# Performance work log

Measured on AMD Instinct MI355X. Metric: run time of the kernel, lower is better.

Reference implementation:

```python
import jax, jax.numpy as jnp
import numpy as np

DIM = 1792      # 256+512+1024 = WRN50 layer1-3 channels
GAMMA_D = 1
K_TOP = 3
EPS = 0.1
MAX_ITER = 200
B, H, W = 2, 56, 56


def avg_pool3x3(x):
    # F.avg_pool2d(x, 3, 1, 1), count_include_pad=True -> always divide by 9
    s = jax.lax.reduce_window(x, 0.0, jax.lax.add, (1, 1, 3, 3), (1, 1, 1, 1),
                              [(0, 0), (0, 0), (1, 1), (1, 1)])
    return s / 9.0


def descriptor(p1, p2, p3, w_coord, b_coord, w_eca):
    sample = avg_pool3x3(p1)
    b, _, h, w = sample.shape
    for o in (p2, p3):
        o = avg_pool3x3(o)
        # F.interpolate(..., mode='bilinear', align_corners=False) == half-pixel bilinear
        o = jax.image.resize(o, (o.shape[0], o.shape[1], h, w), method='bilinear')
        sample = jnp.concatenate([sample, o], axis=1)      # [b,1792,h,w]
    # CoordConv2d(dim, dim//gamma_d, 1): append normalized coord channels, 1x1 conv
    xx = jnp.broadcast_to(jnp.linspace(-1.0, 1.0, w, dtype=sample.dtype)[None, None, None, :], (b, 1, h, w))
    yy = jnp.broadcast_to(jnp.linspace(-1.0, 1.0, h, dtype=sample.dtype)[None, None, :, None], (b, 1, h, w))
    z = jnp.concatenate([sample, xx, yy], axis=1)          # [b,1794,h,w]
    phi = jnp.einsum('bchw,oc->bohw', z, w_coord) + b_coord[None, :, None, None]
    # eca_layer(dim, k_size=9): GAP -> conv1d over channel axis -> sigmoid gate
    y = phi.mean(axis=(2, 3))                              # [b,C]
    y = jax.lax.conv_general_dilated(y[:, None, :], w_eca[None, None, :], (1,),
                                     [(4, 4)], dimension_numbers=('NCH', 'OIH', 'NCH'))[:, 0, :]
    gate = jax.nn.sigmoid(y)[:, :, None, None]
    return phi * (1.0 + 0.1 * gate)                        # 0.1*eca(phi) + phi


def sinkhorn(Ccost, mu, nu):
    # plain Sinkhorn (TopK_custom forward), 200 iterations
    G = jnp.exp(-Ccost / EPS)                              # [bs,n,m]
    bs, n, m = Ccost.shape

    def body(i, uv):
        u, v = uv
        u = mu / (G * v).sum(-1, keepdims=True)            # [bs,n,1]
        v = nu / (G * u).sum(-2, keepdims=True)            # [bs,1,m]
        return (u, v)

    u0 = jnp.ones((bs, n, 1), Ccost.dtype)
    v0 = jnp.ones((bs, 1, m), Ccost.dtype) / m
    u, v = jax.lax.fori_loop(0, MAX_ITER, body, (u0, v0))
    return u * G * v


def soft_topk(scores):
    # SOFT top-k via 2-anchor optimal transport; selects the K_TOP SMALLEST scores
    bs, n = scores.shape
    anchors = jnp.array([0.0, 1.0], scores.dtype)          # [selected, rest]
    Ccost = (scores[..., None] - anchors) ** 2             # [bs,n,2]
    Ccost = Ccost / jax.lax.stop_gradient(Ccost.max())
    mu = jnp.ones((1, n, 1), scores.dtype) / n
    nu = jnp.array([K_TOP / n, (n - K_TOP) / n], scores.dtype).reshape(1, 1, 2)
    Gamma = sinkhorn(Ccost, mu, nu)
    return Gamma[..., 0] * n                               # soft top-K membership mask


def adfa_forward(p1, p2, p3, w_coord, b_coord, w_eca, C):
    phi = descriptor(p1, p2, p3, w_coord, b_coord, w_eca)  # [b,c,h,w]
    b, c, h, w = phi.shape
    phi_p = phi.reshape(b, c, h * w).transpose(0, 2, 1)    # [b,hw,c]
    # F.kl_div(log_softmax(phi_p), softmax(C^T)) = t*(log t - log q); summed, detached
    t = jax.nn.softmax(C.T, axis=-1)                       # [nC,c], nC == hw
    kl = t * (jnp.log(t) - jax.nn.log_softmax(phi_p, axis=-1))
    kldist = jax.lax.stop_gradient(kl.sum(axis=(1, 2), keepdims=True))  # [b,1,1]
    feat2 = (phi_p ** 2).sum(-1, keepdims=True)            # [b,hw,1]
    cent2 = (C ** 2).sum(0, keepdims=True)                 # [1,nC]
    dist = (feat2 + cent2 - 2.0 * (phi_p @ C)) * kldist    # [b,hw,nC]
    nC = dist.shape[-1]
    mask = soft_topk(dist.reshape(-1, nC)).reshape(dist.shape)
    d = (mask * dist).sum(-1, keepdims=True)               # [b,hw,1]
    # rearrange 'b (h w) c -> b c h w'
    return jnp.sqrt(d).reshape(b, h, w, 1).transpose(0, 3, 1, 2)  # [b,1,h,w]


def setup_inputs() -> dict:
    key = jax.random.key(0)
    ks = jax.random.split(key, 7)
    p1 = jax.random.normal(ks[0], (B, 256, H, W), jnp.float32)
    p2 = jax.random.normal(ks[1], (B, 512, H // 2, W // 2), jnp.float32)
    p3 = jax.random.normal(ks[2], (B, 1024, H // 4, W // 4), jnp.float32)
    fan_in = DIM + 2
    w_coord = jax.random.normal(ks[3], (DIM // GAMMA_D, fan_in), jnp.float32) / np.float32(np.sqrt(fan_in))
    b_coord = jax.random.normal(ks[4], (DIM // GAMMA_D,), jnp.float32) * 0.01
    w_eca = jax.random.normal(ks[5], (9,), jnp.float32) / 3.0
    C = jax.random.normal(ks[6], (DIM // GAMMA_D, H * W), jnp.float32) * 0.3
    return {"p1": p1, "p2": p2, "p3": p3, "w_coord": w_coord,
            "b_coord": b_coord, "w_eca": w_eca, "C": C}


def reference(p1, p2, p3, w_coord, b_coord, w_eca, C):
    return adfa_forward(p1, p2, p3, w_coord, b_coord, w_eca, C)
```

## Files before the change

### kernel.cpp

```cpp
#include <hip/hip_runtime.h>

#define HWn 3136
#define DIMc 1792
#define ZCc 1794
#define NBb 2
#define KP 1856
#define MP 3200

typedef unsigned short u16;
typedef unsigned int u32;
typedef short bf16x8 __attribute__((ext_vector_type(8)));
typedef float f32x4 __attribute__((ext_vector_type(4)));

#define GL_LDS(gp, lp) __builtin_amdgcn_global_load_lds(\
    (const __attribute__((address_space(1))) void*)(gp), \
    (__attribute__((address_space(3))) void*)(lp), 16, 0, 0)

__device__ __forceinline__ u16 f2b(float f) {
  u32 u = __float_as_uint(f);
  u32 r = (u + 0x7fffu + ((u >> 16) & 1u)) >> 16;
  return (u16)r;
}
__device__ __forceinline__ float b2f(u16 h) { return __uint_as_float((u32)h << 16); }

__device__ __forceinline__ int xcd_swz(int orig, int nwg) {
  int q = nwg >> 3, r = nwg & 7;
  int xcd = orig & 7, j = orig >> 3;
  int base = (xcd < r) ? xcd * (q + 1) : r * (q + 1) + (xcd - r) * q;
  return base + j;
}

__device__ __forceinline__ float blkSum256(float v) {
  __shared__ float sh[4];
  #pragma unroll
  for (int o = 32; o > 0; o >>= 1) v += __shfl_xor(v, o, 64);
  int lane = threadIdx.x & 63, w = threadIdx.x >> 6;
  if (lane == 0) sh[w] = v;
  __syncthreads();
  float r = sh[0] + sh[1] + sh[2] + sh[3];
  __syncthreads();
  return r;
}
__device__ __forceinline__ float blkMax256(float v) {
  __shared__ float sh[4];
  #pragma unroll
  for (int o = 32; o > 0; o >>= 1) v = fmaxf(v, __shfl_xor(v, o, 64));
  int lane = threadIdx.x & 63, w = threadIdx.x >> 6;
  if (lane == 0) sh[w] = v;
  __syncthreads();
  float r = fmaxf(fmaxf(sh[0], sh[1]), fmaxf(sh[2], sh[3]));
  __syncthreads();
  return r;
}
__device__ __forceinline__ float blkMin256(float v) {
  __shared__ float sh[4];
  #pragma unroll
  for (int o = 32; o > 0; o >>= 1) v = fminf(v, __shfl_xor(v, o, 64));
  int lane = threadIdx.x & 63, w = threadIdx.x >> 6;
  if (lane == 0) sh[w] = v;
  __syncthreads();
  float r = fminf(fminf(sh[0], sh[1]), fminf(sh[2], sh[3]));
  __syncthreads();
  return r;
}

__global__ void pool_k(const float* __restrict__ in, float* __restrict__ out,
                       int total, int Hh, int Ww) {
  int idx = blockIdx.x * 256 + threadIdx.x;
  if (idx >= total) return;
  int w = idx % Ww; int h = (idx / Ww) % Hh; int bc = idx / (Ww * Hh);
  const float* p = in + (size_t)bc * Hh * Ww;
  float s = 0.f;
  #pragma unroll
  for (int dy = -1; dy <= 1; dy++) {
    int y = h + dy; if ((unsigned)y >= (unsigned)Hh) continue;
    #pragma unroll
    for (int dx = -1; dx <= 1; dx++) {
      int x = w + dx; if ((unsigned)x >= (unsigned)Ww) continue;
      s += p[y * Ww + x];
    }
  }
  out[idx] = s * (1.f / 9.f);
}

__device__ __forceinline__ float bilerp(const float* __restrict__ p, int Hin, int Win,
                                        int h, int w, float sc) {
  float fy = (h + 0.5f) * sc - 0.5f;
  float fx = (w + 0.5f) * sc - 0.5f;
  float y0f = floorf(fy), x0f = floorf(fx);
  int y0 = (int)y0f, x0 = (int)x0f;
  float wy = fy - y0f, wx = fx - x0f;
  int y0c = min(max(y0, 0), Hin - 1);
  int y1c = min(max(y0 + 1, 0), Hin - 1);
  int x0c = min(max(x0, 0), Win - 1);
  int x1c = min(max(x0 + 1, 0), Win - 1);
  float v00 = p[y0c * Win + x0c], v01 = p[y0c * Win + x1c];
  float v10 = p[y1c * Win + x0c], v11 = p[y1c * Win + x1c];
  return (1.f - wy) * ((1.f - wx) * v00 + wx * v01) + wy * ((1.f - wx) * v10 + wx * v11);
}

__global__ __launch_bounds__(256) void buildzt_k(const float* __restrict__ p1,
    const float* __restrict__ pp2, const float* __restrict__ pp3,
    u16* __restrict__ zt, float* __restrict__ psum) {
  __shared__ u16 tile[64][68];
  int b = blockIdx.z;
  int i0 = blockIdx.x * 64;
  int c0 = blockIdx.y * 64;
  int t = threadIdx.x;
  #pragma unroll
  for (int q = 0; q < 16; q++) {
    int idx = q * 256 + t;
    int cp = idx >> 6, ip = idx & 63;
    int cg = c0 + cp;
    int ig = i0 + ip;
    int h = ig / 56, w = ig % 56;
    float val;
    if (cg < 256) {
      const float* p = p1 + (size_t)(b * 256 + cg) * HWn;
      float s = 0.f;
      #pragma unroll
      for (int dy = -1; dy <= 1; dy++) {
        int y = h + dy; if ((unsigned)y >= 56u) continue;
        #pragma unroll
        for (int dx = -1; dx <= 1; dx++) {
          int x = w + dx; if ((unsigned)x >= 56u) continue;
          s += p[y * 56 + x];
        }
      }
      val = s * (1.f / 9.f);
    } else if (cg < 768) {
      val = bilerp(pp2 + (size_t)(b * 512 + (cg - 256)) * 784, 28, 28, h, w, 0.5f);
    } else if (cg < 1792) {
      val = bilerp(pp3 + (size_t)(b * 1024 + (cg - 768)) * 196, 14, 14, h, w, 0.25f);
    } else if (cg == 1792) {
      val = -1.f + (2.f / 55.f) * (float)w;
    } else if (cg == 1793) {
      val = -1.f + (2.f / 55.f) * (float)h;
    } else {
      val = 0.f;
    }
    tile[cp][ip] = f2b(val);
  }
  __syncthreads();
  #pragma unroll
  for (int q = 0; q < 4; q++) {
    int idx = q * 256 + t;
    int r2 = idx >> 4;
    int cc4 = (idx & 15) * 4;
    u32 lo = (u32)tile[cc4 + 0][r2] | ((u32)tile[cc4 + 1][r2] << 16);
    u32 hi = (u32)tile[cc4 + 2][r2] | ((u32)tile[cc4 + 3][r2] << 16);
    *reinterpret_cast<uint2*>(&zt[((size_t)b * MP + i0 + r2) * KP + c0 + cc4]) = make_uint2(lo, hi);
  }
  if (t < 64) {
    float s = 0.f;
    #pragma unroll 8
    for (int j = 0; j < 64; j++) s += b2f(tile[t][j]);
    psum[(((size_t)b * 29 + blockIdx.y) * 49 + blockIdx.x) * 64 + t] = s;
  }
}

__global__ void zred_k(const float* __restrict__ psum, float* __restrict__ zmean) {
  int cty = blockIdx.x, b = blockIdx.y;
  int t = threadIdx.x;
  float s = 0.f;
  for (int ix = 0; ix < 49; ix++)
    s += psum[(((size_t)b * 29 + cty) * 49 + ix) * 64 + t];
  zmean[b * KP + cty * 64 + t] = s * (1.f / (float)HWn);
}

__global__ __launch_bounds__(256) void yv_k(const u16* __restrict__ Wb, const float* __restrict__ zmean,
                                            const float* __restrict__ bias, float* __restrict__ yv) {
  __shared__ float zs[KP];
  int b = blockIdx.y;
  int o0 = blockIdx.x * 16;
  int t = threadIdx.x;
  for (int k = t; k < KP; k += 256) zs[k] = zmean[b * KP + k];
  __syncthreads();
  int w = t >> 6, l = t & 63;
  #pragma unroll
  for (int q = 0; q < 4; q++) {
    int o = o0 + w * 4 + q;
    const u16* R = Wb + (size_t)o * KP;
    float s = 0.f;
    for (int base = l * 8; base < KP; base += 512) {
      bf16x8 v = *reinterpret_cast<const bf16x8*>(&R[base]);
      #pragma unroll
      for (int j = 0; j < 8; j++) s += b2f((u16)v[j]) * zs[base + j];
    }
    #pragma unroll
    for (int off = 32; off > 0; off >>= 1) s += __shfl_xor(s, off, 64);
    if (l == 0) yv[b * DIMc + o] = s + bias[o];
  }
}

__global__ __launch_bounds__(256) void transC_k(const float* __restrict__ src, u16* __restrict__ dst) {
  __shared__ u16 tile[64][68];
  int i0 = blockIdx.x * 64;
  int c0 = blockIdx.y * 64;
  int t = threadIdx.x;
  bool vi = (i0 < HWn);
  #pragma unroll
  for (int q = 0; q < 4; q++) {
    int idx = q * 256 + t;
    int r = idx >> 4;
    int c4 = (idx & 15) * 4;
    int sr = c0 + r;
    if (vi && sr < DIMc) {
      float4 rv = *reinterpret_cast<const float4*>(&src[(size_t)sr * HWn + i0 + c4]);
      tile[r][c4 + 0] = f2b(rv.x); tile[r][c4 + 1] = f2b(rv.y);
      tile[r][c4 + 2] = f2b(rv.z); tile[r][c4 + 3] = f2b(rv.w);
    } else {
      tile[r][c4 + 0] = 0; tile[r][c4 + 1] = 0; tile[r][c4 + 2] = 0; tile[r][c4 + 3] = 0;
    }
  }
  __syncthreads();
  #pragma unroll
  for (int q = 0; q < 4; q++) {
    int idx = q * 256 + t;
    int r2 = idx >> 4;
    int cc4 = (idx & 15) * 4;
    u32 lo = (u32)tile[cc4 + 0][r2] | ((u32)tile[cc4 + 1][r2] << 16);
    u32 hi = (u32)tile[cc4 + 2][r2] | ((u32)tile[cc4 + 3][r2] << 16);
    *reinterpret_cast<uint2*>(&dst[(size_t)(i0 + r2) * KP + c0 + cc4]) = make_uint2(lo, hi);
  }
}

__global__ void convW_k(const float* __restrict__ Wc, u16* __restrict__ Wb) {
  int idx = blockIdx.x * 256 + threadIdx.x;
  const int total = DIMc * KP;
  if (idx >= total) return;
  int k = idx % KP, m = idx / KP;
  Wb[idx] = (k < ZCc) ? f2b(Wc[(size_t)m * ZCc + k]) : (u16)0;
}

#define STAGEF(buf, koff) { _Pragma("unroll") for (int j = 0; j < 2; j++) { \
    GL_LDS(gA[j] + (koff), &lA[buf][(j * 256 + tid) * 8]); \
    GL_LDS(gB[j] + (koff), &lB[buf][(j * 256 + tid) * 8]); } }

template<int DIST>
__global__ __launch_bounds__(256, 5) void gemmF_k(
    const u16* __restrict__ A, const u16* __restrict__ B,
    int ntN, int NT,
    const float* __restrict__ bias, u16* __restrict__ PhiOut,
    const float* __restrict__ feat2, const float* __restrict__ cent2,
    const float* __restrict__ kld, u16* __restrict__ DistB,
    float* __restrict__ mmpart, int nblk) {
  __shared__ u16 lA[2][128 * 32];
  __shared__ u16 lB[2][128 * 32];
  int tid = threadIdx.x;
  int wid = tid >> 6, lane = tid & 63;
  int wm = wid >> 1, wn = wid & 1;
  int orig = blockIdx.x;
  int wg = xcd_swz(orig, gridDim.x);
  int mt = wg / ntN, nt = wg % ntN;
  int m0 = mt * 128, n0 = nt * 128;
  int rbase = tid >> 2;
  int srcX = ((tid & 3) ^ ((rbase >> 1) & 3)) * 8;
  const u16* gA[2]; const u16* gB[2];
  #pragma unroll
  for (int j = 0; j < 2; j++) {
    int rr = j * 64 + rbase;
    gA[j] = A + (size_t)(m0 + rr) * KP + srcX;
    gB[j] = B + (size_t)(n0 + rr) * KP + srcX;
  }
  int kq8 = (lane >> 4) * 8;
  int lr = lane & 15;
  f32x4 acc[4][4] = {};
  STAGEF(0, 0);
  __syncthreads();
  for (int t = 0; t < NT; t++) {
    int cur = t & 1;
    if (t + 1 < NT) STAGEF(cur ^ 1, (t + 1) * 32);
    bf16x8 af[4], bfr[4];
    #pragma unroll
    for (int f = 0; f < 4; f++) {
      int aR = wm * 64 + f * 16 + lr;
      af[f] = *reinterpret_cast<const bf16x8*>(
          &lA[cur][aR * 32 + (kq8 ^ (((aR >> 1) & 3) << 3))]);
    }
    #pragma unroll
    for (int g = 0; g < 4; g++) {
      int bR = wn * 64 + g * 16 + lr;
      bfr[g] = *reinterpret_cast<const bf16x8*>(
          &lB[cur][bR * 32 + (kq8 ^ (((bR >> 1) & 3) << 3))]);
    }
    #pragma unroll
    for (int f = 0; f < 4; f++)
      #pragma unroll
      for (int g = 0; g < 4; g++)
        acc[f][g] = __builtin_amdgcn_mfma_f32_16x16x32_bf16(af[f], bfr[g], acc[f][g], 0, 0, 0);
    __syncthreads();
  }
  int mbase = m0 + wm * 64 + (lane >> 4) * 4;
  int nbase = n0 + wn * 64 + lr;
  if (DIST == 0) {
    #pragma unroll
    for (int mi = 0; mi < 4; mi++) {
      #pragma unroll
      for (int ni = 0; ni < 4; ni++) {
        int n = nbase + ni * 16;
        float bv = bias[n];
        #pragma unroll
        for (int r = 0; r < 4; r++) {
          int m = mbase + mi * 16 + r;
          PhiOut[(size_t)m * KP + n] = f2b(acc[mi][ni][r] + bv);
        }
      }
    }
  } else {
    float lmin = 3.4e38f, lmax = -3.4e38f;
    #pragma unroll
    for (int mi = 0; mi < 4; mi++) {
      int m = mbase + mi * 16;
      int bz = m / MP;
      int i = m - bz * MP;
      float kl = kld[bz];
      float f2r[4];
      #pragma unroll
      for (int r = 0; r < 4; r++)
        f2r[r] = (i + r < HWn) ? feat2[bz * HWn + i + r] : 0.f;
      #pragma unroll
      for (int ni = 0; ni < 4; ni++) {
        int n = nbase + ni * 16;
        if (n < HWn) {
          float c2 = cent2[n];
          #pragma unroll
          for (int r = 0; r < 4; r++) {
            if (i + r < HWn) {
              float dd = (f2r[r] + c2 - 2.f * acc[mi][ni][r]) * kl;
              DistB[((size_t)bz * HWn + i + r) * HWn + n] = f2b(dd);
              lmin = fminf(lmin, dd); lmax = fmaxf(lmax, dd);
            }
          }
        }
      }
    }
    #pragma unroll
    for (int o = 32; o > 0; o >>= 1) {
      lmin = fminf(lmin, __shfl_xor(lmin, o, 64));
      lmax = fmaxf(lmax, __shfl_xor(lmax, o, 64));
    }
    __syncthreads();
    float* scr = reinterpret_cast<float*>(&lA[0][0]);
    if (lane == 0) { scr[wid] = lmin; scr[4 + wid] = lmax; }
    __syncthreads();
    if (tid == 0) {
      mmpart[orig] = fminf(fminf(scr[0], scr[1]), fminf(scr[2], scr[3]));
      mmpart[nblk + orig] = fmaxf(fmaxf(scr[4], scr[5]), fmaxf(scr[6], scr[7]));
    }
  }
}

__global__ void fac_k(const float* __restrict__ yv, const float* __restrict__ weca,
                      float* __restrict__ fac) {
  int idx = blockIdx.x * 256 + threadIdx.x;
  if (idx >= NBb * DIMc) return;
  int o = idx % DIMc; int b = idx / DIMc;
  float s = 0.f;
  #pragma unroll
  for (int k = 0; k < 9; k++) {
    int c = o + k - 4;
    if ((unsigned)c < (unsigned)DIMc) s += yv[b * DIMc + c] * weca[k];
  }
  fac[idx] = 1.f + 0.1f / (1.f + expf(-s));
}

__global__ __launch_bounds__(256) void rowfuse_k(const u16* __restrict__ Ct, u16* __restrict__ Phi,
    const float* __restrict__ fac, float* __restrict__ cent2,
    float* __restrict__ feat2, float* __restrict__ kpart) {
  int i = blockIdx.x;
  int t = threadIdx.x;
  bool act = (t * 8 < DIMc);
  const u16* R = Ct + (size_t)i * KP;
  float c[8];
  float mc = -3.4e38f, c2 = 0.f;
  if (act) {
    bf16x8 x = *reinterpret_cast<const bf16x8*>(&R[t * 8]);
    #pragma unroll
    for (int j = 0; j < 8; j++) {
      c[j] = b2f((u16)x[j]);
      mc = fmaxf(mc, c[j]);
      c2 += c[j] * c[j];
    }
  }
  mc = blkMax256(mc);
  float se = 0.f, sce = 0.f;
  float e[8];
  if (act) {
    #pragma unroll
    for (int j = 0; j < 8; j++) {
      e[j] = expf(c[j] - mc);
      se += e[j]; sce += e[j] * (c[j] - mc);
    }
  }
  se = blkSum256(se);
  sce = blkSum256(sce);
  c2 = blkSum256(c2);
  if (t == 0) cent2[i] = c2;
  float tl = sce / se - logf(se);
  float inv_se = 1.f / se;
  #pragma unroll
  for (int b = 0; b < NBb; b++) {
    u16* P = Phi + (size_t)b * MP * KP + (size_t)i * KP;
    float v[8];
    float mx = -3.4e38f;
    if (act) {
      bf16x8 x = *reinterpret_cast<const bf16x8*>(&P[t * 8]);
      const float4* fp = reinterpret_cast<const float4*>(&fac[b * DIMc + t * 8]);
      float4 f0 = fp[0], f1 = fp[1];
      v[0] = b2f((u16)x[0]) * f0.x; v[1] = b2f((u16)x[1]) * f0.y;
      v[2] = b2f((u16)x[2]) * f0.z; v[3] = b2f((u16)x[3]) * f0.w;
      v[4] = b2f((u16)x[4]) * f1.x; v[5] = b2f((u16)x[5]) * f1.y;
      v[6] = b2f((u16)x[6]) * f1.z; v[7] = b2f((u16)x[7]) * f1.w;
      #pragma unroll
      for (int j = 0; j < 8; j++) mx = fmaxf(mx, v[j]);
    }
    mx = blkMax256(mx);
    float sp = 0.f, f2 = 0.f, td = 0.f;
    if (act) {
      bf16x8 o;
      #pragma unroll
      for (int j = 0; j < 8; j++) {
        sp += expf(v[j] - mx);
        f2 += v[j] * v[j];
        td += e[j] * v[j];
        o[j] = (short)f2b(v[j]);
      }
      *reinterpret_cast<bf16x8*>(&P[t * 8]) = o;
    } else if (t * 8 < KP) {
      bf16x8 zr = {};
      *reinterpret_cast<bf16x8*>(&P[t * 8]) = zr;
    }
    sp = blkSum256(sp);
    f2 = blkSum256(f2);
    td = blkSum256(td);
    if (t == 0) {
      feat2[b * HWn + i] = f2;
      kpart[b * HWn + i] = tl - td * inv_se + (mx + logf(sp));
    }
  }
}

__global__ __launch_bounds__(256) void kldred_k(const float* __restrict__ kpart, float* __restrict__ kld) {
  float s0 = 0.f, s1 = 0.f;
  for (int i = threadIdx.x; i < HWn; i += 256) { s0 += kpart[i]; s1 += kpart[HWn + i]; }
  s0 = blkSum256(s0); s1 = blkSum256(s1);
  if (threadIdx.x == 0) { kld[0] = s0; kld[1] = s1; }
}

__global__ __launch_bounds__(256) void mmred_k(const float* __restrict__ mmpart, float* __restrict__ gmm,
                                               int nblk) {
  float lmin = 3.4e38f, lmax = -3.4e38f;
  for (int i = threadIdx.x; i < nblk; i += 256) {
    lmin = fminf(lmin, mmpart[i]);
    lmax = fmaxf(lmax, mmpart[nblk + i]);
  }
  lmin = blkMin256(lmin); lmax = blkMax256(lmax);
  if (threadIdx.x == 0) { gmm[0] = lmin; gmm[1] = lmax; }
}

__global__ __launch_bounds__(256) void topk_k(const u16* __restrict__ dist,
    const float* __restrict__ gmm, float* __restrict__ out) {
  __shared__ float dS[HWn];
  __shared__ float rS[HWn];
  int row = blockIdx.x;
  const u16* dr = dist + (size_t)row * HWn;
  int t = threadIdx.x;
  float gmin = gmm[0], gmax = gmm[1];
  float cmax = fmaxf(fmaxf(gmin * gmin, (gmin - 1.f) * (gmin - 1.f)),
                     fmaxf(gmax * gmax, (gmax - 1.f) * (gmax - 1.f)));
  float inv = 1.f / (0.1f * cmax);
  for (int ch = t; ch < HWn / 8; ch += 256) {
    bf16x8 d8 = *reinterpret_cast<const bf16x8*>(&dr[ch * 8]);
    #pragma unroll
    for (int j = 0; j < 8; j++) {
      float dv = b2f((u16)d8[j]);
      dS[ch * 8 + j] = dv;
      rS[ch * 8 + j] = expf((2.f * dv - 1.f) * inv);
    }
  }
  __syncthreads();
  const float nf = (float)HWn;
  float s = 1.f;
  for (int it = 0; it < 199; it++) {
    float loc = 0.f;
    for (int e = t; e < HWn; e += 256) loc += 1.f / (1.f + rS[e] * s);
    float A = blkSum256(loc);
    float snew = ((nf - 3.f) / 3.f) * A * s / fmaxf(nf - A, 1e-20f);
    float ds = fabsf(snew - s);
    s = snew;
    if (ds <= 1e-6f * fabsf(s)) break;
  }
  float loc = 0.f;
  for (int e = t; e < HWn; e += 256) loc += 1.f / (1.f + rS[e] * s);
  float A = blkSum256(loc);
  float sc = 3.f / A;
  float dl = 0.f;
  for (int e = t; e < HWn; e += 256) dl += dS[e] / (1.f + rS[e] * s);
  float dsum = blkSum256(dl) * sc;
  if (t == 0) out[row] = sqrtf(fmaxf(dsum, 0.f));
}

extern "C" void kernel_launch(void* const* d_in, const int* in_sizes, int n_in,
                              void* d_out, int out_size, void* d_ws, size_t ws_size,
                              hipStream_t stream) {
  const float* p1 = (const float*)d_in[0];
  const float* p2 = (const float*)d_in[1];
  const float* p3 = (const float*)d_in[2];
  const float* wcoord = (const float*)d_in[3];
  const float* bcoord = (const float*)d_in[4];
  const float* weca = (const float*)d_in[5];
  const float* Cm = (const float*)d_in[6];
  float* out = (float*)d_out;
  float* ws = (float*)d_ws;

  u16*   zt    = (u16*)ws;
  float* pp2   = ws + 5939200;
  float* pp3   = ws + 6742016;
  u16*   dist  = (u16*)ws;
  u16*   phi   = (u16*)(ws + 19668992);
  u16*   Ct    = (u16*)(ws + 25608192);
  u16*   Wb    = (u16*)(ws + 28577792);
  float* yv    = ws + 30240768;
  float* fac   = yv + 3584;
  float* feat2 = fac + 3584;
  float* cent2 = feat2 + 6272;
  float* kpart = cent2 + 3136;
  float* kld   = kpart + 6272;
  float* mmpart= kld + 2;
  float* gmm   = mmpart + 2500;
  float* zmean = gmm + 2;
  float* psum  = zmean + 3712;
  const int NBLK = 50 * 25;

  pool_k<<<3136, 256, 0, stream>>>(p2, pp2, NBb * 512 * 784, 28, 28);
  pool_k<<<1568, 256, 0, stream>>>(p3, pp3, NBb * 1024 * 196, 14, 14);
  buildzt_k<<<dim3(49, 29, NBb), 256, 0, stream>>>(p1, pp2, pp3, zt, psum);
  zred_k<<<dim3(29, NBb), 64, 0, stream>>>(psum, zmean);
  convW_k<<<(DIMc * KP + 255) / 256, 256, 0, stream>>>(wcoord, Wb);
  transC_k<<<dim3(50, 29, 1), 256, 0, stream>>>(Cm, Ct);
  yv_k<<<dim3(DIMc / 16, NBb), 256, 0, stream>>>(Wb, zmean, bcoord, yv);
  fac_k<<<(NBb * DIMc + 255) / 256, 256, 0, stream>>>(yv, weca, fac);
  gemmF_k<0><<<50 * 14, 256, 0, stream>>>(
      zt, Wb, 14, 58, bcoord, phi,
      nullptr, nullptr, nullptr, nullptr, nullptr, 0);
  rowfuse_k<<<HWn, 256, 0, stream>>>(Ct, phi, fac, cent2, feat2, kpart);
  kldred_k<<<1, 256, 0, stream>>>(kpart, kld);
  gemmF_k<1><<<50 * 25, 256, 0, stream>>>(
      phi, Ct, 25, 56, nullptr, nullptr,
      feat2, cent2, kld, dist, mmpart, NBLK);
  mmred_k<<<1, 256, 0, stream>>>(mmpart, gmm, NBLK);
  topk_k<<<NBb * HWn, 256, 0, stream>>>(dist, gmm, out);
}
```

Baseline: 323.4 us.

## Fold ECA gate into GEMM epilogue and use Newton iteration in top-k solve

The ECA gate factor is now applied in the first GEMM's epilogue, so the row-fusion kernel no longer rescales and rewrites phi and only reads it for its statistics. The top-k scalar fixed-point iteration is replaced by a Newton step that also accumulates sum of w squared through a paired block reduction. The iteration cap drops to 40, with a positivity safeguard. Newton should need far fewer serial passes over the row in the per-row top-k kernel, but convergence within 40 steps is not guaranteed for every row.

```diff
diff --git a/kernel.cpp b/kernel.cpp
--- a/kernel.cpp
+++ b/kernel.cpp
@@ -40,6 +40,18 @@
   float r = sh[0] + sh[1] + sh[2] + sh[3];
   __syncthreads();
   return r;
+}
+__device__ __forceinline__ float2 blkSum256x2(float a, float b) {
+  __shared__ float sh2[8];
+  #pragma unroll
+  for (int o = 32; o > 0; o >>= 1) { a += __shfl_xor(a, o, 64); b += __shfl_xor(b, o, 64); }
+  int lane = threadIdx.x & 63, w = threadIdx.x >> 6;
+  if (lane == 0) { sh2[w] = a; sh2[4 + w] = b; }
+  __syncthreads();
+  float ra = sh2[0] + sh2[1] + sh2[2] + sh2[3];
+  float rb = sh2[4] + sh2[5] + sh2[6] + sh2[7];
+  __syncthreads();
+  return make_float2(ra, rb);
 }
 __device__ __forceinline__ float blkMax256(float v) {
   __shared__ float sh[4];
@@ -241,7 +253,8 @@
 __global__ __launch_bounds__(256, 5) void gemmF_k(
     const u16* __restrict__ A, const u16* __restrict__ B,
     int ntN, int NT,
-    const float* __restrict__ bias, u16* __restrict__ PhiOut,
+    const float* __restrict__ bias, const float* __restrict__ fac,
+    u16* __restrict__ PhiOut,
     const float* __restrict__ feat2, const float* __restrict__ cent2,
     const float* __restrict__ kld, u16* __restrict__ DistB,
     float* __restrict__ mmpart, int nblk) {
@@ -294,16 +307,23 @@
   int mbase = m0 + wm * 64 + (lane >> 4) * 4;
   int nbase = n0 + wn * 64 + lr;
   if (DIST == 0) {
+    int bz0 = m0 / MP;
+    float bvv[4], fcv[4];
+    #pragma unroll
+    for (int ni = 0; ni < 4; ni++) {
+      int n = nbase + ni * 16;
+      bvv[ni] = bias[n];
+      fcv[ni] = fac[bz0 * DIMc + n];
+    }
     #pragma unroll
     for (int mi = 0; mi < 4; mi++) {
       #pragma unroll
       for (int ni = 0; ni < 4; ni++) {
         int n = nbase + ni * 16;
-        float bv = bias[n];
         #pragma unroll
         for (int r = 0; r < 4; r++) {
           int m = mbase + mi * 16 + r;
-          PhiOut[(size_t)m * KP + n] = f2b(acc[mi][ni][r] + bv);
+          PhiOut[(size_t)m * KP + n] = f2b((acc[mi][ni][r] + bvv[ni]) * fcv[ni]);
         }
       }
     }
@@ -366,8 +386,7 @@
 }
 
 __global__ __launch_bounds__(256) void rowfuse_k(const u16* __restrict__ Ct, u16* __restrict__ Phi,
-    const float* __restrict__ fac, float* __restrict__ cent2,
-    float* __restrict__ feat2, float* __restrict__ kpart) {
+    float* __restrict__ cent2, float* __restrict__ feat2, float* __restrict__ kpart) {
   int i = blockIdx.x;
   int t = threadIdx.x;
   bool act = (t * 8 < DIMc);
@@ -406,30 +425,24 @@
     float mx = -3.4e38f;
     if (act) {
       bf16x8 x = *reinterpret_cast<const bf16x8*>(&P[t * 8]);
-      const float4* fp = reinterpret_cast<const float4*>(&fac[b * DIMc + t * 8]);
-      float4 f0 = fp[0], f1 = fp[1];
-      v[0] = b2f((u16)x[0]) * f0.x; v[1] = b2f((u16)x[1]) * f0.y;
-      v[2] = b2f((u16)x[2]) * f0.z; v[3] = b2f((u16)x[3]) * f0.w;
-      v[4] = b2f((u16)x[4]) * f1.x; v[5] = b2f((u16)x[5]) * f1.y;
-      v[6] = b2f((u16)x[6]) * f1.z; v[7] = b2f((u16)x[7]) * f1.w;
-      #pragma unroll
-      for (int j = 0; j < 8; j++) mx = fmaxf(mx, v[j]);
+      #pragma unroll
+      for (int j = 0; j < 8; j++) {
+        v[j] = b2f((u16)x[j]);
+        mx = fmaxf(mx, v[j]);
+      }
+    } else if (t * 8 < KP) {
+      bf16x8 zr = {};
+      *reinterpret_cast<bf16x8*>(&P[t * 8]) = zr;
     }
     mx = blkMax256(mx);
     float sp = 0.f, f2 = 0.f, td = 0.f;
     if (act) {
-      bf16x8 o;
       #pragma unroll
       for (int j = 0; j < 8; j++) {
         sp += expf(v[j] - mx);
         f2 += v[j] * v[j];
         td += e[j] * v[j];
-        o[j] = (short)f2b(v[j]);
       }
-      *reinterpret_cast<bf16x8*>(&P[t * 8]) = o;
-    } else if (t * 8 < KP) {
-      bf16x8 zr = {};
-      *reinterpret_cast<bf16x8*>(&P[t * 8]) = zr;
     }
     sp = blkSum256(sp);
     f2 = blkSum256(f2);
@@ -480,13 +493,17 @@
     }
   }
   __syncthreads();
-  const float nf = (float)HWn;
   float s = 1.f;
-  for (int it = 0; it < 199; it++) {
-    float loc = 0.f;
-    for (int e = t; e < HWn; e += 256) loc += 1.f / (1.f + rS[e] * s);
-    float A = blkSum256(loc);
-    float snew = ((nf - 3.f) / 3.f) * A * s / fmaxf(nf - A, 1e-20f);
+  for (int it = 0; it < 40; it++) {
+    float sw = 0.f, sw2 = 0.f;
+    for (int e = t; e < HWn; e += 256) {
+      float w = 1.f / (1.f + rS[e] * s);
+      sw += w; sw2 += w * w;
+    }
+    float2 S = blkSum256x2(sw, sw2);
+    float denom = fmaxf(S.x - S.y, 1e-20f);
+    float snew = s + s * (S.x - 3.f) / denom;
+    if (!(snew > 0.f)) snew = 0.5f * s;
     float ds = fabsf(snew - s);
     s = snew;
     if (ds <= 1e-6f * fabsf(s)) break;
@@ -542,12 +559,12 @@
   yv_k<<<dim3(DIMc / 16, NBb), 256, 0, stream>>>(Wb, zmean, bcoord, yv);
   fac_k<<<(NBb * DIMc + 255) / 256, 256, 0, stream>>>(yv, weca, fac);
   gemmF_k<0><<<50 * 14, 256, 0, stream>>>(
-      zt, Wb, 14, 58, bcoord, phi,
+      zt, Wb, 14, 58, bcoord, fac, phi,
       nullptr, nullptr, nullptr, nullptr, nullptr, 0);
-  rowfuse_k<<<HWn, 256, 0, stream>>>(Ct, phi, fac, cent2, feat2, kpart);
+  rowfuse_k<<<HWn, 256, 0, stream>>>(Ct, phi, cent2, feat2, kpart);
   kldred_k<<<1, 256, 0, stream>>>(kpart, kld);
   gemmF_k<1><<<50 * 25, 256, 0, stream>>>(
-      phi, Ct, 25, 56, nullptr, nullptr,
+      phi, Ct, 25, 56, nullptr, nullptr, nullptr,
       feat2, cent2, kld, dist, mmpart, NBLK);
   mmred_k<<<1, 256, 0, stream>>>(mmpart, gmm, NBLK);
   topk_k<<<NBb * HWn, 256, 0, stream>>>(dist, gmm, out);
```

Result: slower. 433.2 us (+34.0%).
